# Performance work log

Measured on AMD Instinct MI355X. Metric: run time of the kernel, lower is better.

## Reference

```python
import jax, jax.numpy as jnp
import numpy as np

N_USER = 100000
N_ITEM = 50000
E = 1600000
D_USER = 128
D_ITEM = 64
H = 256


def setup_inputs() -> dict:
    key = jax.random.key(0)
    ks = jax.random.split(key, 20)
    w = lambda k, shape: (jax.random.normal(k, shape, jnp.float32) * 0.05)
    return {
        "x_user": jax.random.normal(ks[0], (N_USER, D_USER), jnp.float32),
        "x_item": jax.random.normal(ks[1], (N_ITEM, D_ITEM), jnp.float32),
        "edge_ui_src": jax.random.randint(ks[2], (E,), 0, N_USER, jnp.int32),
        "edge_ui_dst": jax.random.randint(ks[3], (E,), 0, N_ITEM, jnp.int32),
        "edge_iu_src": jax.random.randint(ks[4], (E,), 0, N_ITEM, jnp.int32),
        "edge_iu_dst": jax.random.randint(ks[5], (E,), 0, N_USER, jnp.int32),
        # layer 1 (per edge type): lin_l (src_dim->H, with bias), lin_r (dst_dim->H, no bias)
        "W1l_ui": w(ks[6], (H, D_USER)), "b1_ui": w(ks[7], (H,)), "W1r_ui": w(ks[8], (H, D_ITEM)),
        "W1l_iu": w(ks[9], (H, D_ITEM)), "b1_iu": w(ks[10], (H,)), "W1r_iu": w(ks[11], (H, D_USER)),
        # layer 2 (H -> H)
        "W2l_ui": w(ks[12], (H, H)), "b2_ui": w(ks[13], (H,)), "W2r_ui": w(ks[14], (H, H)),
        "W2l_iu": w(ks[15], (H, H)), "b2_iu": w(ks[16], (H,)), "W2r_iu": w(ks[17], (H, H)),
    }


def _sage_conv(x_src, x_dst, src, dst, Wl, b, Wr, n_dst):
    """PyG SAGEConv (aggr='mean', root_weight=True): lin_l(mean_j x_src[j]) + lin_r(x_dst)."""
    msg = x_src[src]                                                     # [E, Fs] gather
    s = jax.ops.segment_sum(msg, dst, num_segments=n_dst)                # [n_dst, Fs]
    cnt = jax.ops.segment_sum(jnp.ones((src.shape[0], 1), x_src.dtype), dst, num_segments=n_dst)
    mean = jnp.where(cnt > 0, s / jnp.maximum(cnt, 1.0), 0.0)            # isolated dst -> 0
    return mean @ Wl.T + b + x_dst @ Wr.T


def reference(x_user, x_item, edge_ui_src, edge_ui_dst, edge_iu_src, edge_iu_dst,
              W1l_ui, b1_ui, W1r_ui, W1l_iu, b1_iu, W1r_iu,
              W2l_ui, b2_ui, W2r_ui, W2l_iu, b2_iu, W2r_iu):
    # layer 1: one conv per edge type; to_hetero sums per dst type (single contributor here)
    h_item = _sage_conv(x_user, x_item, edge_ui_src, edge_ui_dst, W1l_ui, b1_ui, W1r_ui, N_ITEM)
    h_user = _sage_conv(x_item, x_user, edge_iu_src, edge_iu_dst, W1l_iu, b1_iu, W1r_iu, N_USER)
    h_item = jax.nn.relu(h_item)
    h_user = jax.nn.relu(h_user)
    # layer 2 (no activation after last layer in PyG BasicGNN)
    out_item = _sage_conv(h_user, h_item, edge_ui_src, edge_ui_dst, W2l_ui, b2_ui, W2r_ui, N_ITEM)
    out_user = _sage_conv(h_item, h_user, edge_iu_src, edge_iu_dst, W2l_iu, b2_iu, W2r_iu, N_USER)
    return out_user, out_item
```

## Files before the change

### kernel.cpp

```cpp
#include <hip/hip_runtime.h>


typedef unsigned short u16;
typedef unsigned int u32;
typedef short bf16x8 __attribute__((ext_vector_type(8)));
typedef float f32x4 __attribute__((ext_vector_type(4)));

constexpr int HDIM = 256;
constexpr int RB = 128;
constexpr int MAXB = 784;
constexpr int CHUNK = 4096;


__device__ __forceinline__ float lo2f(u32 v) { union { u32 i; float f; } x; x.i = v << 16; return x.f; }
__device__ __forceinline__ float hi2f(u32 v) { union { u32 i; float f; } x; x.i = v & 0xffff0000u; return x.f; }
__device__ __forceinline__ float bf2f(u16 v) { union { u32 i; float f; } x; x.i = ((u32)v) << 16; return x.f; }
__device__ __forceinline__ u16 f2bf(float f) {
    union { float f; u32 i; } x; x.f = f;
    return (u16)((x.i + 0x7fffu + ((x.i >> 16) & 1u)) >> 16);
}
__device__ __forceinline__ u32 pack2(float a, float b) {
    return (u32)f2bf(a) | ((u32)f2bf(b) << 16);
}

__device__ __forceinline__ void gload16(const void* g, void* l) {
    __builtin_amdgcn_global_load_lds(
        (const __attribute__((address_space(1))) unsigned int*)g,
        (__attribute__((address_space(3))) unsigned int*)l, 16, 0, 0);
}


__global__ void hist_kernel(const int* __restrict__ dst, int n, int* __restrict__ cnt) {
    int i = blockIdx.x * 256 + threadIdx.x;
    if (i < n) atomicAdd(&cnt[dst[i]], 1);
}

__global__ void block_reduce_kernel(const int* __restrict__ cnt, int n, int* __restrict__ sums) {
    __shared__ int sdata[256];
    int b = blockIdx.x, t = threadIdx.x;
    int v = 0;
#pragma unroll
    for (int j = 0; j < 4; j++) {
        int idx = b * 1024 + j * 256 + t;
        if (idx < n) v += cnt[idx];
    }
    sdata[t] = v;
    __syncthreads();
    for (int s = 128; s > 0; s >>= 1) {
        if (t < s) sdata[t] += sdata[t + s];
        __syncthreads();
    }
    if (t == 0) sums[b] = sdata[0];
}

__global__ void scan_sums_kernel(const int* __restrict__ sums, int* __restrict__ offs, int B) {
    if (blockIdx.x == 0 && threadIdx.x == 0) {
        int a = 0;
        for (int i = 0; i < B; i++) { offs[i] = a; a += sums[i]; }
    }
}

__global__ void block_scan_write_kernel(const int* cnt, int n, const int* __restrict__ offs,
                                        int* __restrict__ rp, int* cursor, int total) {
    __shared__ int sdata[1024];
    int b = blockIdx.x, t = threadIdx.x;
    int idx = b * 1024 + t;
    int v = (idx < n) ? cnt[idx] : 0;
    sdata[t] = v;
    __syncthreads();
    for (int s = 1; s < 1024; s <<= 1) {
        int x = (t >= s) ? sdata[t - s] : 0;
        __syncthreads();
        sdata[t] += x;
        __syncthreads();
    }
    if (idx < n) {
        int excl = sdata[t] - v + offs[b];
        rp[idx] = excl;
        cursor[idx] = excl;
    }
    if (b == 0 && t == 0) rp[n] = total;
}

__global__ void bucket_init_kernel(const int* __restrict__ rp, int n, int nb,
                                   int* __restrict__ bcur) {
    int b = blockIdx.x * 256 + threadIdx.x;
    if (b < nb) {
        int row = b * RB;
        bcur[b] = rp[row < n ? row : n];
    }
}

__global__ __launch_bounds__(256) void binned_scatter(const int* __restrict__ src,
                                                      const int* __restrict__ dst, int E,
                                                      int nb, int* __restrict__ bcur,
                                                      uint2* __restrict__ pairs) {
    __shared__ int lcnt[MAXB];
    __shared__ int lbase[MAXB];
    const int t = threadIdx.x;
    const int chunk = blockIdx.x * CHUNK;

    for (int b = t; b < nb; b += 256) lcnt[b] = 0;
    __syncthreads();

    u32 ss[CHUNK / 256], dd[CHUNK / 256];
#pragma unroll
    for (int j = 0; j < CHUNK / 256; j++) {
        int i = chunk + j * 256 + t;
        if (i < E) {
            ss[j] = (u32)src[i];
            dd[j] = (u32)dst[i];
            atomicAdd(&lcnt[dd[j] >> 7], 1);
        } else {
            ss[j] = 0; dd[j] = 0;
        }
    }
    __syncthreads();

    for (int b = t; b < nb; b += 256) {
        int c = lcnt[b];
        lbase[b] = (c > 0) ? atomicAdd(&bcur[b], c) : 0;
    }
    __syncthreads();
    for (int b = t; b < nb; b += 256) lcnt[b] = 0;
    __syncthreads();

#pragma unroll
    for (int j = 0; j < CHUNK / 256; j++) {
        int i = chunk + j * 256 + t;
        if (i < E) {
            int b = (int)(dd[j] >> 7);
            int r = atomicAdd(&lcnt[b], 1);
            pairs[(size_t)lbase[b] + r] = make_uint2(ss[j], dd[j]);
        }
    }
}

__global__ __launch_bounds__(256) void bucket_fill(const uint2* __restrict__ pairs,
                                                   const int* __restrict__ rp, int n,
                                                   int* __restrict__ col) {
    __shared__ int lcur[RB];
    const int b = blockIdx.x;
    const int r0 = b * RB;
    const int rend = (r0 + RB < n) ? r0 + RB : n;
    const int t = threadIdx.x;
    if (t < RB) {
        int row = r0 + t;
        lcur[t] = (row < rend) ? rp[row] : 0;
    }
    __syncthreads();
    const int e0 = rp[r0];
    const int e1 = rp[rend];
    for (int j = e0 + t; j < e1; j += 256) {
        uint2 e = pairs[j];
        int p = atomicAdd(&lcur[e.y - (u32)r0], 1);
        col[p] = (int)e.x;
    }
}


__global__ void f32_to_bf16_kernel(const float* __restrict__ in, u16* __restrict__ out, int n4) {
    int i = blockIdx.x * 256 + threadIdx.x;
    if (i < n4) {
        float4 v = ((const float4*)in)[i];
        ((uint2*)out)[i] = make_uint2(pack2(v.x, v.y), pack2(v.z, v.w));
    }
}


template <int F>
__global__ __launch_bounds__(256) void agg_mean(const u16* __restrict__ src,
                                                const int* __restrict__ rp,
                                                const int* __restrict__ col,
                                                u16* __restrict__ out, int n_dst) {
    constexpr int G = F / 8;
    constexpr int R = 64 / G;
    const int lane = threadIdx.x & 63;
    const int d = blockIdx.x * 4 + (threadIdx.x >> 6);
    if (d >= n_dst) return;
    const int sub = lane / G;
    const int li = lane & (G - 1);
    const int e0 = rp[d], e1 = rp[d + 1];
    const size_t lo = (size_t)li * 8;

    float a[8] = {0.f, 0.f, 0.f, 0.f, 0.f, 0.f, 0.f, 0.f};
    auto add8 = [&](uint4 v) {
        a[0] += lo2f(v.x); a[1] += hi2f(v.x);
        a[2] += lo2f(v.y); a[3] += hi2f(v.y);
        a[4] += lo2f(v.z); a[5] += hi2f(v.z);
        a[6] += lo2f(v.w); a[7] += hi2f(v.w);
    };

    int ebase = e0;
    for (; ebase + 4 * R <= e1; ebase += 4 * R) {
        const int e = ebase + sub;
        int c0 = col[e];
        int c1 = col[e + R];
        int c2 = col[e + 2 * R];
        int c3 = col[e + 3 * R];
        uint4 v0 = *(const uint4*)(src + (size_t)c0 * F + lo);
        uint4 v1 = *(const uint4*)(src + (size_t)c1 * F + lo);
        uint4 v2 = *(const uint4*)(src + (size_t)c2 * F + lo);
        uint4 v3 = *(const uint4*)(src + (size_t)c3 * F + lo);
        add8(v0); add8(v1); add8(v2); add8(v3);
    }
    for (int e = ebase + sub; e < e1; e += R) {
        int c = col[e];
        uint4 v = *(const uint4*)(src + (size_t)c * F + lo);
        add8(v);
    }

#pragma unroll
    for (int m = G; m < 64; m <<= 1) {
#pragma unroll
        for (int j = 0; j < 8; j++) a[j] += __shfl_xor(a[j], m, 64);
    }

    const int deg = e1 - e0;
    const float inv = (deg > 0) ? 1.f / (float)deg : 0.f;
    if (lane < G) {
        uint4 w;
        w.x = pack2(a[0] * inv, a[1] * inv);
        w.y = pack2(a[2] * inv, a[3] * inv);
        w.z = pack2(a[4] * inv, a[5] * inv);
        w.w = pack2(a[6] * inv, a[7] * inv);
        *(uint4*)(out + (size_t)d * F + lo) = w;
    }
}


template <int KA, int KB, bool RELU, bool OUT_BF16>
__global__ __launch_bounds__(256, 3) void gemm_tile(const u16* __restrict__ A,
                                                    const u16* __restrict__ X,
                                                    const u16* __restrict__ WA,
                                                    const u16* __restrict__ WB,
                                                    const float* __restrict__ bias,
                                                    float* __restrict__ outF,
                                                    u16* __restrict__ outB, int M) {
    constexpr int KT = KA + KB;
    constexpr int NKT = KT / 32;
    __shared__ __align__(16) u16 Al[128 * 32];
    __shared__ __align__(16) u16 Wl[128 * 32];

    const int nwg = gridDim.x;
    const int b = blockIdx.x;
    const int q = nwg >> 3, r = nwg & 7;
    const int xcd = b & 7, within = b >> 3;
    const int logical = (xcd < r ? xcd * (q + 1) : r * (q + 1) + (xcd - r) * q) + within;
    const int mb = logical >> 1;
    const int nb = logical & 1;
    const int row0 = mb * 128;
    const int ncol0 = nb * 128;

    const int tid = threadIdx.x;
    const int lane = tid & 63;
    const int wid = tid >> 6;
    const int wr = wid >> 1;
    const int wc = wid & 1;
    const int ml = lane & 15;
    const int ql = lane >> 4;
    const int lrow4 = lane >> 2;
    const int lcol8 = (lane & 3) * 8;

    f32x4 acc[4][4];
#pragma unroll
    for (int m = 0; m < 4; m++)
#pragma unroll
        for (int n = 0; n < 4; n++) acc[m][n] = {0.f, 0.f, 0.f, 0.f};

    const int s0 = wid * 2;

#pragma unroll
    for (int kt = 0; kt < NKT; ++kt) {
        const int kk = kt * 32;
#pragma unroll
        for (int j = 0; j < 2; ++j) {
            const int s = s0 + j;
            int gr = row0 + s * 16 + lrow4;
            gr = (gr < M) ? gr : (M - 1);
            const u16* gp = (kk < KA) ? (A + (size_t)gr * KA + (kk + lcol8))
                                      : (X + (size_t)gr * KB + (kk - KA + lcol8));
            gload16(gp, &Al[s * 512]);
        }
#pragma unroll
        for (int j = 0; j < 2; ++j) {
            const int s = s0 + j;
            const int gn = ncol0 + s * 16 + lrow4;
            const u16* gp = (kk < KA) ? (WA + (size_t)gn * KA + (kk + lcol8))
                                      : (WB + (size_t)gn * KB + (kk - KA + lcol8));
            gload16(gp, &Wl[s * 512]);
        }
        __syncthreads();

        bf16x8 af[4], wf[4];
#pragma unroll
        for (int m = 0; m < 4; m++)
            af[m] = *(const bf16x8*)&Al[(wr * 64 + m * 16 + ml) * 32 + ql * 8];
#pragma unroll
        for (int n = 0; n < 4; n++)
            wf[n] = *(const bf16x8*)&Wl[(wc * 64 + n * 16 + ml) * 32 + ql * 8];
#pragma unroll
        for (int m = 0; m < 4; m++)
#pragma unroll
            for (int n = 0; n < 4; n++)
                acc[m][n] = __builtin_amdgcn_mfma_f32_16x16x32_bf16(af[m], wf[n], acc[m][n], 0, 0, 0);
        __syncthreads();
    }

#pragma unroll
    for (int n = 0; n < 4; n++) {
        const int gcol = ncol0 + wc * 64 + n * 16 + ml;
        const float bv = bias[gcol];
#pragma unroll
        for (int m = 0; m < 4; m++) {
            const int gr0 = row0 + wr * 64 + m * 16 + ql * 4;
#pragma unroll
            for (int rr = 0; rr < 4; rr++) {
                const int grow = gr0 + rr;
                if (grow >= M) continue;
                float v = acc[m][n][rr] + bv;
                if (RELU) v = fmaxf(v, 0.f);
                if (OUT_BF16) outB[(size_t)grow * HDIM + gcol] = f2bf(v);
                else          outF[(size_t)grow * HDIM + gcol] = v;
            }
        }
    }
}


extern "C" void kernel_launch(void* const* d_in, const int* in_sizes, int n_in,
                              void* d_out, int out_size, void* d_ws, size_t ws_size,
                              hipStream_t stream) {
    const float* x_user = (const float*)d_in[0];
    const float* x_item = (const float*)d_in[1];
    const int* eui_src = (const int*)d_in[2];
    const int* eui_dst = (const int*)d_in[3];
    const int* eiu_src = (const int*)d_in[4];
    const int* eiu_dst = (const int*)d_in[5];
    const float* W1l_ui = (const float*)d_in[6];
    const float* b1_ui  = (const float*)d_in[7];
    const float* W1r_ui = (const float*)d_in[8];
    const float* W1l_iu = (const float*)d_in[9];
    const float* b1_iu  = (const float*)d_in[10];
    const float* W1r_iu = (const float*)d_in[11];
    const float* W2l_ui = (const float*)d_in[12];
    const float* b2_ui  = (const float*)d_in[13];
    const float* W2r_ui = (const float*)d_in[14];
    const float* W2l_iu = (const float*)d_in[15];
    const float* b2_iu  = (const float*)d_in[16];
    const float* W2r_iu = (const float*)d_in[17];

    const int DU = 128, DI = 64;
    const int NU = in_sizes[0] / DU;
    const int NI = in_sizes[1] / DI;
    const int E  = in_sizes[2];

    char* base = (char*)d_ws;
    size_t off = 0;
    auto carve = [&](size_t bytes) -> char* {
        char* p = base + off;
        off += (bytes + 255) & ~(size_t)255;
        return p;
    };
    int* cnt_i  = (int*)carve((size_t)NI * 4);
    int* cnt_u  = (int*)carve((size_t)NU * 4);
    int* rp_i   = (int*)carve((size_t)(NI + 1) * 4);
    int* rp_u   = (int*)carve((size_t)(NU + 1) * 4);
    int* col_ui = (int*)carve((size_t)E * 4);
    int* col_iu = (int*)carve((size_t)E * 4);
    int* bsum   = (int*)carve(1024 * 4);
    int* boff   = (int*)carve(1024 * 4);
    int* bcur_i = (int*)carve(MAXB * 4);
    int* bcur_u = (int*)carve(MAXB * 4);
    u16* W1l_ui_b = (u16*)carve((size_t)HDIM * DU * 2);
    u16* W1r_ui_b = (u16*)carve((size_t)HDIM * DI * 2);
    u16* W1l_iu_b = (u16*)carve((size_t)HDIM * DI * 2);
    u16* W1r_iu_b = (u16*)carve((size_t)HDIM * DU * 2);
    u16* W2l_ui_b = (u16*)carve((size_t)HDIM * HDIM * 2);
    u16* W2r_ui_b = (u16*)carve((size_t)HDIM * HDIM * 2);
    u16* W2l_iu_b = (u16*)carve((size_t)HDIM * HDIM * 2);
    u16* W2r_iu_b = (u16*)carve((size_t)HDIM * HDIM * 2);
    char* slot1 = carve((size_t)NU * DU * 2);
    u16* x_user_b = (u16*)slot1;
    u16* B_i      = (u16*)slot1;
    char* slotB = carve((size_t)NU * HDIM * 2);
    u16* x_item_b = (u16*)slotB;
    u16* A_i      = (u16*)(slotB + (size_t)NI * DI * 2);
    u16* A_u      = (u16*)(slotB + (size_t)NI * DI * 2 + (size_t)NI * DU * 2);
    u16* B_u      = (u16*)slotB;
    u16* h_item_b = (u16*)carve((size_t)NI * HDIM * 2);
    u16* h_user_b = (u16*)carve((size_t)NU * HDIM * 2);

    uint2* pairs = (uint2*)h_user_b;

    float* out_user = (float*)d_out;
    float* out_item = (float*)d_out + (size_t)NU * HDIM;

    hipMemsetAsync(cnt_i, 0, (size_t)NI * 4, stream);
    hipMemsetAsync(cnt_u, 0, (size_t)NU * 4, stream);
    int egrid = (E + 255) / 256;
    hist_kernel<<<egrid, 256, 0, stream>>>(eui_dst, E, cnt_i);
    hist_kernel<<<egrid, 256, 0, stream>>>(eiu_dst, E, cnt_u);
    int Bi = (NI + 1023) / 1024, Bu = (NU + 1023) / 1024;
    block_reduce_kernel<<<Bi, 256, 0, stream>>>(cnt_i, NI, bsum);
    scan_sums_kernel<<<1, 64, 0, stream>>>(bsum, boff, Bi);
    block_scan_write_kernel<<<Bi, 1024, 0, stream>>>(cnt_i, NI, boff, rp_i, cnt_i, E);
    block_reduce_kernel<<<Bu, 256, 0, stream>>>(cnt_u, NU, bsum);
    scan_sums_kernel<<<1, 64, 0, stream>>>(bsum, boff, Bu);
    block_scan_write_kernel<<<Bu, 1024, 0, stream>>>(cnt_u, NU, boff, rp_u, cnt_u, E);

    const int nb_i = (NI + RB - 1) / RB;
    const int nb_u = (NU + RB - 1) / RB;
    const int sgrid = (E + CHUNK - 1) / CHUNK;
    bucket_init_kernel<<<(nb_i + 255) / 256, 256, 0, stream>>>(rp_i, NI, nb_i, bcur_i);
    binned_scatter<<<sgrid, 256, 0, stream>>>(eui_src, eui_dst, E, nb_i, bcur_i, pairs);
    bucket_fill<<<nb_i, 256, 0, stream>>>(pairs, rp_i, NI, col_ui);
    bucket_init_kernel<<<(nb_u + 255) / 256, 256, 0, stream>>>(rp_u, NU, nb_u, bcur_u);
    binned_scatter<<<sgrid, 256, 0, stream>>>(eiu_src, eiu_dst, E, nb_u, bcur_u, pairs);
    bucket_fill<<<nb_u, 256, 0, stream>>>(pairs, rp_u, NU, col_iu);

    auto conv = [&](const float* in, u16* outp, size_t n) {
        int n4 = (int)(n / 4);
        f32_to_bf16_kernel<<<(n4 + 255) / 256, 256, 0, stream>>>(in, outp, n4);
    };
    conv(x_user, x_user_b, (size_t)NU * DU);
    conv(x_item, x_item_b, (size_t)NI * DI);
    conv(W1l_ui, W1l_ui_b, (size_t)HDIM * DU);
    conv(W1r_ui, W1r_ui_b, (size_t)HDIM * DI);
    conv(W1l_iu, W1l_iu_b, (size_t)HDIM * DI);
    conv(W1r_iu, W1r_iu_b, (size_t)HDIM * DU);
    conv(W2l_ui, W2l_ui_b, (size_t)HDIM * HDIM);
    conv(W2r_ui, W2r_ui_b, (size_t)HDIM * HDIM);
    conv(W2l_iu, W2l_iu_b, (size_t)HDIM * HDIM);
    conv(W2r_iu, W2r_iu_b, (size_t)HDIM * HDIM);

    agg_mean<128><<<(NI + 3) / 4, 256, 0, stream>>>(x_user_b, rp_i, col_ui, A_i, NI);
    agg_mean<64> <<<(NU + 3) / 4, 256, 0, stream>>>(x_item_b, rp_u, col_iu, A_u, NU);
    {
        int gi = ((NI + 127) / 128) * 2;
        int gu = ((NU + 127) / 128) * 2;
        gemm_tile<128, 64, true, true><<<gi, 256, 0, stream>>>(
            A_i, x_item_b, W1l_ui_b, W1r_ui_b, b1_ui, nullptr, h_item_b, NI);
        gemm_tile<64, 128, true, true><<<gu, 256, 0, stream>>>(
            A_u, x_user_b, W1l_iu_b, W1r_iu_b, b1_iu, nullptr, h_user_b, NU);
    }

    agg_mean<256><<<(NI + 3) / 4, 256, 0, stream>>>(h_user_b, rp_i, col_ui, B_i, NI);
    agg_mean<256><<<(NU + 3) / 4, 256, 0, stream>>>(h_item_b, rp_u, col_iu, B_u, NU);
    {
        int gi = ((NI + 127) / 128) * 2;
        int gu = ((NU + 127) / 128) * 2;
        gemm_tile<256, 256, false, false><<<gi, 256, 0, stream>>>(
            B_i, h_item_b, W2l_ui_b, W2r_ui_b, b2_ui, out_item, nullptr, NI);
        gemm_tile<256, 256, false, false><<<gu, 256, 0, stream>>>(
            B_u, h_user_b, W2l_iu_b, W2r_iu_b, b2_iu, out_user, nullptr, NU);
    }
}
```

Before: 965.1 us.

## Fuse CSR build, conversions and layer-2 aggregation into fewer kernels

Replaces the per-node histogram plus multi-kernel scan with bucket-level counting, a single-block bucket scan, and row offsets computed inside the bucket fill. Both edge types are handled in one combined launch per stage, using separate pair buffers. The ten fp32-to-bf16 conversions become one grid-stride kernel, and the two layer-2 aggregations share one launch. The aggregation loop gains an 8-way unrolled gather. The aim is fewer launches, less scan work and more gathers in flight, at the cost of more registers and an assumption that the bucket count fits in 1024.

```diff
diff --git a/kernel.cpp b/kernel.cpp
--- a/kernel.cpp
+++ b/kernel.cpp
@@ -14,7 +14,6 @@
 
 __device__ __forceinline__ float lo2f(u32 v) { union { u32 i; float f; } x; x.i = v << 16; return x.f; }
 __device__ __forceinline__ float hi2f(u32 v) { union { u32 i; float f; } x; x.i = v & 0xffff0000u; return x.f; }
-__device__ __forceinline__ float bf2f(u16 v) { union { u32 i; float f; } x; x.i = ((u32)v) << 16; return x.f; }
 __device__ __forceinline__ u16 f2bf(float f) {
     union { float f; u32 i; } x; x.f = f;
     return (u16)((x.i + 0x7fffu + ((x.i >> 16) & 1u)) >> 16);
@@ -30,77 +29,81 @@
 }
 
 
-__global__ void hist_kernel(const int* __restrict__ dst, int n, int* __restrict__ cnt) {
-    int i = blockIdx.x * 256 + threadIdx.x;
-    if (i < n) atomicAdd(&cnt[dst[i]], 1);
-}
-
-__global__ void block_reduce_kernel(const int* __restrict__ cnt, int n, int* __restrict__ sums) {
-    __shared__ int sdata[256];
-    int b = blockIdx.x, t = threadIdx.x;
-    int v = 0;
-#pragma unroll
-    for (int j = 0; j < 4; j++) {
-        int idx = b * 1024 + j * 256 + t;
-        if (idx < n) v += cnt[idx];
-    }
-    sdata[t] = v;
-    __syncthreads();
-    for (int s = 128; s > 0; s >>= 1) {
-        if (t < s) sdata[t] += sdata[t + s];
-        __syncthreads();
-    }
-    if (t == 0) sums[b] = sdata[0];
-}
-
-__global__ void scan_sums_kernel(const int* __restrict__ sums, int* __restrict__ offs, int B) {
-    if (blockIdx.x == 0 && threadIdx.x == 0) {
-        int a = 0;
-        for (int i = 0; i < B; i++) { offs[i] = a; a += sums[i]; }
-    }
-}
-
-__global__ void block_scan_write_kernel(const int* cnt, int n, const int* __restrict__ offs,
-                                        int* __restrict__ rp, int* cursor, int total) {
-    __shared__ int sdata[1024];
-    int b = blockIdx.x, t = threadIdx.x;
-    int idx = b * 1024 + t;
-    int v = (idx < n) ? cnt[idx] : 0;
-    sdata[t] = v;
-    __syncthreads();
-    for (int s = 1; s < 1024; s <<= 1) {
-        int x = (t >= s) ? sdata[t - s] : 0;
-        __syncthreads();
-        sdata[t] += x;
-        __syncthreads();
-    }
-    if (idx < n) {
-        int excl = sdata[t] - v + offs[b];
-        rp[idx] = excl;
-        cursor[idx] = excl;
-    }
-    if (b == 0 && t == 0) rp[n] = total;
-}
-
-__global__ void bucket_init_kernel(const int* __restrict__ rp, int n, int nb,
-                                   int* __restrict__ bcur) {
-    int b = blockIdx.x * 256 + threadIdx.x;
-    if (b < nb) {
-        int row = b * RB;
-        bcur[b] = rp[row < n ? row : n];
-    }
-}
-
-__global__ __launch_bounds__(256) void binned_scatter(const int* __restrict__ src,
-                                                      const int* __restrict__ dst, int E,
-                                                      int nb, int* __restrict__ bcur,
-                                                      uint2* __restrict__ pairs) {
+__global__ __launch_bounds__(256) void bucket_count(const int* __restrict__ dst0, int nb0,
+                                                    int* __restrict__ bc0,
+                                                    const int* __restrict__ dst1, int nb1,
+                                                    int* __restrict__ bc1,
+                                                    int E, int sgrid) {
+    __shared__ int lcnt[MAXB];
+    int b = blockIdx.x;
+    const int* dst; int nb; int* bc;
+    if (b < sgrid) { dst = dst0; nb = nb0; bc = bc0; }
+    else           { b -= sgrid; dst = dst1; nb = nb1; bc = bc1; }
+    const int t = threadIdx.x;
+    for (int i = t; i < nb; i += 256) lcnt[i] = 0;
+    __syncthreads();
+    const int base = b * CHUNK;
+#pragma unroll
+    for (int j = 0; j < CHUNK / 256; j++) {
+        int i = base + j * 256 + t;
+        if (i < E) atomicAdd(&lcnt[dst[i] >> 7], 1);
+    }
+    __syncthreads();
+    for (int i = t; i < nb; i += 256) {
+        int c = lcnt[i];
+        if (c) atomicAdd(&bc[i], c);
+    }
+}
+
+__global__ __launch_bounds__(1024) void bucket_scan(const int* __restrict__ bc0,
+                                                    int* __restrict__ base0,
+                                                    int* __restrict__ bcur0, int nb0,
+                                                    const int* __restrict__ bc1,
+                                                    int* __restrict__ base1,
+                                                    int* __restrict__ bcur1, int nb1) {
+    __shared__ int s[1024];
+    const int t = threadIdx.x;
+    int own = (t < nb0) ? bc0[t] : 0;
+    s[t] = own;
+    __syncthreads();
+    for (int st = 1; st < 1024; st <<= 1) {
+        int v = (t >= st) ? s[t - st] : 0;
+        __syncthreads();
+        s[t] += v;
+        __syncthreads();
+    }
+    if (t < nb0) { int ex = s[t] - own; base0[t] = ex; bcur0[t] = ex; }
+    if (t == 0) base0[nb0] = s[1023];
+    __syncthreads();
+    own = (t < nb1) ? bc1[t] : 0;
+    s[t] = own;
+    __syncthreads();
+    for (int st = 1; st < 1024; st <<= 1) {
+        int v = (t >= st) ? s[t - st] : 0;
+        __syncthreads();
+        s[t] += v;
+        __syncthreads();
+    }
+    if (t < nb1) { int ex = s[t] - own; base1[t] = ex; bcur1[t] = ex; }
+    if (t == 0) base1[nb1] = s[1023];
+}
+
+__global__ __launch_bounds__(256) void binned_scatter2(
+    const int* __restrict__ src0, const int* __restrict__ dst0, int nb0,
+    int* __restrict__ bcur0, uint2* __restrict__ pairs0,
+    const int* __restrict__ src1, const int* __restrict__ dst1, int nb1,
+    int* __restrict__ bcur1, uint2* __restrict__ pairs1,
+    int E, int sgrid) {
     __shared__ int lcnt[MAXB];
     __shared__ int lbase[MAXB];
+    int b = blockIdx.x;
+    const int *src, *dst; int nb; int* bcur; uint2* pairs;
+    if (b < sgrid) { src = src0; dst = dst0; nb = nb0; bcur = bcur0; pairs = pairs0; }
+    else           { b -= sgrid; src = src1; dst = dst1; nb = nb1; bcur = bcur1; pairs = pairs1; }
     const int t = threadIdx.x;
-    const int chunk = blockIdx.x * CHUNK;
-
-    for (int b = t; b < nb; b += 256) lcnt[b] = 0;
+    const int chunk = b * CHUNK;
+
+    for (int i = t; i < nb; i += 256) lcnt[i] = 0;
     __syncthreads();
 
     u32 ss[CHUNK / 256], dd[CHUNK / 256];
@@ -117,66 +120,91 @@
     }
     __syncthreads();
 
-    for (int b = t; b < nb; b += 256) {
-        int c = lcnt[b];
-        lbase[b] = (c > 0) ? atomicAdd(&bcur[b], c) : 0;
-    }
-    __syncthreads();
-    for (int b = t; b < nb; b += 256) lcnt[b] = 0;
+    for (int i = t; i < nb; i += 256) {
+        int c = lcnt[i];
+        lbase[i] = (c > 0) ? atomicAdd(&bcur[i], c) : 0;
+    }
+    __syncthreads();
+    for (int i = t; i < nb; i += 256) lcnt[i] = 0;
     __syncthreads();
 
 #pragma unroll
     for (int j = 0; j < CHUNK / 256; j++) {
         int i = chunk + j * 256 + t;
         if (i < E) {
-            int b = (int)(dd[j] >> 7);
-            int r = atomicAdd(&lcnt[b], 1);
-            pairs[(size_t)lbase[b] + r] = make_uint2(ss[j], dd[j]);
+            int bb = (int)(dd[j] >> 7);
+            int r = atomicAdd(&lcnt[bb], 1);
+            pairs[(size_t)lbase[bb] + r] = make_uint2(ss[j], dd[j]);
         }
     }
 }
 
-__global__ __launch_bounds__(256) void bucket_fill(const uint2* __restrict__ pairs,
-                                                   const int* __restrict__ rp, int n,
-                                                   int* __restrict__ col) {
+__global__ __launch_bounds__(256) void bucket_fill2(
+    const uint2* __restrict__ pairs0, const int* __restrict__ base0, int nb0, int n0,
+    int* __restrict__ rp0, int* __restrict__ col0,
+    const uint2* __restrict__ pairs1, const int* __restrict__ base1, int n1,
+    int* __restrict__ rp1, int* __restrict__ col1) {
+    __shared__ int rcnt[RB];
+    __shared__ int excl[RB];
     __shared__ int lcur[RB];
-    const int b = blockIdx.x;
+    int b = blockIdx.x;
+    const uint2* pairs; const int* bb; int n; int* rp; int* col;
+    if (b < nb0) { pairs = pairs0; bb = base0; n = n0; rp = rp0; col = col0; }
+    else         { b -= nb0; pairs = pairs1; bb = base1; n = n1; rp = rp1; col = col1; }
+    const int t = threadIdx.x;
     const int r0 = b * RB;
-    const int rend = (r0 + RB < n) ? r0 + RB : n;
-    const int t = threadIdx.x;
+    const int e0 = bb[b], e1 = bb[b + 1];
+
+    if (t < RB) rcnt[t] = 0;
+    __syncthreads();
+    for (int j = e0 + t; j < e1; j += 256) atomicAdd(&rcnt[pairs[j].y & (RB - 1)], 1);
+    __syncthreads();
+    int own = (t < RB) ? rcnt[t] : 0;
+    if (t < RB) excl[t] = own;
+    __syncthreads();
+    for (int st = 1; st < RB; st <<= 1) {
+        int v = (t < RB && t >= st) ? excl[t - st] : 0;
+        __syncthreads();
+        if (t < RB) excl[t] += v;
+        __syncthreads();
+    }
     if (t < RB) {
+        int ex = e0 + excl[t] - own;
         int row = r0 + t;
-        lcur[t] = (row < rend) ? rp[row] : 0;
-    }
-    __syncthreads();
-    const int e0 = rp[r0];
-    const int e1 = rp[rend];
+        if (row < n) rp[row] = ex;
+        lcur[t] = ex;
+    }
+    if (t == 0 && r0 + RB >= n) rp[n] = e1;
+    __syncthreads();
     for (int j = e0 + t; j < e1; j += 256) {
         uint2 e = pairs[j];
-        int p = atomicAdd(&lcur[e.y - (u32)r0], 1);
+        int p = atomicAdd(&lcur[e.y & (RB - 1)], 1);
         col[p] = (int)e.x;
     }
 }
 
 
-__global__ void f32_to_bf16_kernel(const float* __restrict__ in, u16* __restrict__ out, int n4) {
-    int i = blockIdx.x * 256 + threadIdx.x;
-    if (i < n4) {
-        float4 v = ((const float4*)in)[i];
-        ((uint2*)out)[i] = make_uint2(pack2(v.x, v.y), pack2(v.z, v.w));
+struct ConvSeg { const float* in; u16* out; u32 n4; u32 pad; };
+struct ConvArgs { ConvSeg s[10]; u32 tot; };
+
+__global__ __launch_bounds__(256) void multi_convert(ConvArgs a) {
+    for (u32 i = blockIdx.x * 256 + threadIdx.x; i < a.tot; i += gridDim.x * 256) {
+        u32 r = i;
+        int sg = 0;
+        while (r >= a.s[sg].n4) { r -= a.s[sg].n4; sg++; }
+        float4 v = ((const float4*)a.s[sg].in)[r];
+        ((uint2*)a.s[sg].out)[r] = make_uint2(pack2(v.x, v.y), pack2(v.z, v.w));
     }
 }
 
 
 template <int F>
-__global__ __launch_bounds__(256) void agg_mean(const u16* __restrict__ src,
-                                                const int* __restrict__ rp,
-                                                const int* __restrict__ col,
-                                                u16* __restrict__ out, int n_dst) {
+__device__ __forceinline__ void agg_row(const u16* __restrict__ src, const int* __restrict__ rp,
+                                        const int* __restrict__ col, u16* __restrict__ out,
+                                        int n_dst, int d) {
     constexpr int G = F / 8;
     constexpr int R = 64 / G;
     const int lane = threadIdx.x & 63;
-    const int d = blockIdx.x * 4 + (threadIdx.x >> 6);
     if (d >= n_dst) return;
     const int sub = lane / G;
     const int li = lane & (G - 1);
@@ -192,21 +220,28 @@
     };
 
     int ebase = e0;
+    for (; ebase + 8 * R <= e1; ebase += 8 * R) {
+        int c[8];
+#pragma unroll
+        for (int k = 0; k < 8; k++) c[k] = col[ebase + sub + k * R];
+        uint4 v[8];
+#pragma unroll
+        for (int k = 0; k < 8; k++) v[k] = *(const uint4*)(src + (size_t)c[k] * F + lo);
+#pragma unroll
+        for (int k = 0; k < 8; k++) add8(v[k]);
+    }
     for (; ebase + 4 * R <= e1; ebase += 4 * R) {
-        const int e = ebase + sub;
-        int c0 = col[e];
-        int c1 = col[e + R];
-        int c2 = col[e + 2 * R];
-        int c3 = col[e + 3 * R];
-        uint4 v0 = *(const uint4*)(src + (size_t)c0 * F + lo);
-        uint4 v1 = *(const uint4*)(src + (size_t)c1 * F + lo);
-        uint4 v2 = *(const uint4*)(src + (size_t)c2 * F + lo);
-        uint4 v3 = *(const uint4*)(src + (size_t)c3 * F + lo);
-        add8(v0); add8(v1); add8(v2); add8(v3);
+        int c[4];
+#pragma unroll
+        for (int k = 0; k < 4; k++) c[k] = col[ebase + sub + k * R];
+        uint4 v[4];
+#pragma unroll
+        for (int k = 0; k < 4; k++) v[k] = *(const uint4*)(src + (size_t)c[k] * F + lo);
+#pragma unroll
+        for (int k = 0; k < 4; k++) add8(v[k]);
     }
     for (int e = ebase + sub; e < e1; e += R) {
-        int c = col[e];
-        uint4 v = *(const uint4*)(src + (size_t)c * F + lo);
+        uint4 v = *(const uint4*)(src + (size_t)col[e] * F + lo);
         add8(v);
     }
 
@@ -226,6 +261,24 @@
         w.w = pack2(a[6] * inv, a[7] * inv);
         *(uint4*)(out + (size_t)d * F + lo) = w;
     }
+}
+
+template <int F>
+__global__ __launch_bounds__(256) void agg_mean(const u16* __restrict__ src,
+                                                const int* __restrict__ rp,
+                                                const int* __restrict__ col,
+                                                u16* __restrict__ out, int n_dst) {
+    agg_row<F>(src, rp, col, out, n_dst, blockIdx.x * 4 + (threadIdx.x >> 6));
+}
+
+__global__ __launch_bounds__(256) void agg_mean256_dual(
+    const u16* __restrict__ src0, const int* __restrict__ rp0, const int* __restrict__ col0,
+    u16* __restrict__ out0, int n0, int g0,
+    const u16* __restrict__ src1, const int* __restrict__ rp1, const int* __restrict__ col1,
+    u16* __restrict__ out1, int n1) {
+    const int b = blockIdx.x;
+    if (b < g0) agg_row<256>(src0, rp0, col0, out0, n0, b * 4 + (threadIdx.x >> 6));
+    else        agg_row<256>(src1, rp1, col1, out1, n1, (b - g0) * 4 + (threadIdx.x >> 6));
 }
 
 
@@ -362,14 +415,15 @@
         off += (bytes + 255) & ~(size_t)255;
         return p;
     };
-    int* cnt_i  = (int*)carve((size_t)NI * 4);
-    int* cnt_u  = (int*)carve((size_t)NU * 4);
     int* rp_i   = (int*)carve((size_t)(NI + 1) * 4);
     int* rp_u   = (int*)carve((size_t)(NU + 1) * 4);
     int* col_ui = (int*)carve((size_t)E * 4);
     int* col_iu = (int*)carve((size_t)E * 4);
-    int* bsum   = (int*)carve(1024 * 4);
-    int* boff   = (int*)carve(1024 * 4);
+    int* bc     = (int*)carve((size_t)2 * MAXB * 4);
+    int* bc_i   = bc;
+    int* bc_u   = bc + MAXB;
+    int* base_i = (int*)carve((size_t)(MAXB + 1) * 4);
+    int* base_u = (int*)carve((size_t)(MAXB + 1) * 4);
     int* bcur_i = (int*)carve(MAXB * 4);
     int* bcur_u = (int*)carve(MAXB * 4);
     u16* W1l_ui_b = (u16*)carve((size_t)HDIM * DU * 2);
@@ -391,48 +445,46 @@
     u16* h_item_b = (u16*)carve((size_t)NI * HDIM * 2);
     u16* h_user_b = (u16*)carve((size_t)NU * HDIM * 2);
 
-    uint2* pairs = (uint2*)h_user_b;
+    uint2* pairs_i = (uint2*)h_user_b;
+    uint2* pairs_u = (uint2*)(h_user_b + (size_t)E * 4);
 
     float* out_user = (float*)d_out;
     float* out_item = (float*)d_out + (size_t)NU * HDIM;
-
-    hipMemsetAsync(cnt_i, 0, (size_t)NI * 4, stream);
-    hipMemsetAsync(cnt_u, 0, (size_t)NU * 4, stream);
-    int egrid = (E + 255) / 256;
-    hist_kernel<<<egrid, 256, 0, stream>>>(eui_dst, E, cnt_i);
-    hist_kernel<<<egrid, 256, 0, stream>>>(eiu_dst, E, cnt_u);
-    int Bi = (NI + 1023) / 1024, Bu = (NU + 1023) / 1024;
-    block_reduce_kernel<<<Bi, 256, 0, stream>>>(cnt_i, NI, bsum);
-    scan_sums_kernel<<<1, 64, 0, stream>>>(bsum, boff, Bi);
-    block_scan_write_kernel<<<Bi, 1024, 0, stream>>>(cnt_i, NI, boff, rp_i, cnt_i, E);
-    block_reduce_kernel<<<Bu, 256, 0, stream>>>(cnt_u, NU, bsum);
-    scan_sums_kernel<<<1, 64, 0, stream>>>(bsum, boff, Bu);
-    block_scan_write_kernel<<<Bu, 1024, 0, stream>>>(cnt_u, NU, boff, rp_u, cnt_u, E);
 
     const int nb_i = (NI + RB - 1) / RB;
     const int nb_u = (NU + RB - 1) / RB;
     const int sgrid = (E + CHUNK - 1) / CHUNK;
-    bucket_init_kernel<<<(nb_i + 255) / 256, 256, 0, stream>>>(rp_i, NI, nb_i, bcur_i);
-    binned_scatter<<<sgrid, 256, 0, stream>>>(eui_src, eui_dst, E, nb_i, bcur_i, pairs);
-    bucket_fill<<<nb_i, 256, 0, stream>>>(pairs, rp_i, NI, col_ui);
-    bucket_init_kernel<<<(nb_u + 255) / 256, 256, 0, stream>>>(rp_u, NU, nb_u, bcur_u);
-    binned_scatter<<<sgrid, 256, 0, stream>>>(eiu_src, eiu_dst, E, nb_u, bcur_u, pairs);
-    bucket_fill<<<nb_u, 256, 0, stream>>>(pairs, rp_u, NU, col_iu);
-
-    auto conv = [&](const float* in, u16* outp, size_t n) {
-        int n4 = (int)(n / 4);
-        f32_to_bf16_kernel<<<(n4 + 255) / 256, 256, 0, stream>>>(in, outp, n4);
-    };
-    conv(x_user, x_user_b, (size_t)NU * DU);
-    conv(x_item, x_item_b, (size_t)NI * DI);
-    conv(W1l_ui, W1l_ui_b, (size_t)HDIM * DU);
-    conv(W1r_ui, W1r_ui_b, (size_t)HDIM * DI);
-    conv(W1l_iu, W1l_iu_b, (size_t)HDIM * DI);
-    conv(W1r_iu, W1r_iu_b, (size_t)HDIM * DU);
-    conv(W2l_ui, W2l_ui_b, (size_t)HDIM * HDIM);
-    conv(W2r_ui, W2r_ui_b, (size_t)HDIM * HDIM);
-    conv(W2l_iu, W2l_iu_b, (size_t)HDIM * HDIM);
-    conv(W2r_iu, W2r_iu_b, (size_t)HDIM * HDIM);
+
+    hipMemsetAsync(bc, 0, (size_t)2 * MAXB * 4, stream);
+    bucket_count<<<2 * sgrid, 256, 0, stream>>>(eui_dst, nb_i, bc_i, eiu_dst, nb_u, bc_u, E, sgrid);
+    bucket_scan<<<1, 1024, 0, stream>>>(bc_i, base_i, bcur_i, nb_i, bc_u, base_u, bcur_u, nb_u);
+    binned_scatter2<<<2 * sgrid, 256, 0, stream>>>(
+        eui_src, eui_dst, nb_i, bcur_i, pairs_i,
+        eiu_src, eiu_dst, nb_u, bcur_u, pairs_u, E, sgrid);
+    bucket_fill2<<<nb_i + nb_u, 256, 0, stream>>>(
+        pairs_i, base_i, nb_i, NI, rp_i, col_ui,
+        pairs_u, base_u, NU, rp_u, col_iu);
+
+    {
+        ConvArgs ca;
+        auto seg = [&](int i, const float* in, u16* outp, size_t n) {
+            ca.s[i].in = in; ca.s[i].out = outp; ca.s[i].n4 = (u32)(n / 4); ca.s[i].pad = 0;
+        };
+        seg(0, x_user, x_user_b, (size_t)NU * DU);
+        seg(1, x_item, x_item_b, (size_t)NI * DI);
+        seg(2, W2l_ui, W2l_ui_b, (size_t)HDIM * HDIM);
+        seg(3, W2r_ui, W2r_ui_b, (size_t)HDIM * HDIM);
+        seg(4, W2l_iu, W2l_iu_b, (size_t)HDIM * HDIM);
+        seg(5, W2r_iu, W2r_iu_b, (size_t)HDIM * HDIM);
+        seg(6, W1l_ui, W1l_ui_b, (size_t)HDIM * DU);
+        seg(7, W1r_ui, W1r_ui_b, (size_t)HDIM * DI);
+        seg(8, W1l_iu, W1l_iu_b, (size_t)HDIM * DI);
+        seg(9, W1r_iu, W1r_iu_b, (size_t)HDIM * DU);
+        u32 tot = 0;
+        for (int i = 0; i < 10; i++) tot += ca.s[i].n4;
+        ca.tot = tot;
+        multi_convert<<<2048, 256, 0, stream>>>(ca);
+    }
 
     agg_mean<128><<<(NI + 3) / 4, 256, 0, stream>>>(x_user_b, rp_i, col_ui, A_i, NI);
     agg_mean<64> <<<(NU + 3) / 4, 256, 0, stream>>>(x_item_b, rp_u, col_iu, A_u, NU);
@@ -445,8 +497,13 @@
             A_u, x_user_b, W1l_iu_b, W1r_iu_b, b1_iu, nullptr, h_user_b, NU);
     }
 
-    agg_mean<256><<<(NI + 3) / 4, 256, 0, stream>>>(h_user_b, rp_i, col_ui, B_i, NI);
-    agg_mean<256><<<(NU + 3) / 4, 256, 0, stream>>>(h_item_b, rp_u, col_iu, B_u, NU);
+    {
+        int gi = (NI + 3) / 4;
+        int gu = (NU + 3) / 4;
+        agg_mean256_dual<<<gi + gu, 256, 0, stream>>>(
+            h_user_b, rp_i, col_ui, B_i, NI, gi,
+            h_item_b, rp_u, col_iu, B_u, NU);
+    }
     {
         int gi = ((NI + 127) / 128) * 2;
         int gu = ((NU + 127) / 128) * 2;
```

After: 824.8 us. -14.5%, faster.
